# Optimization experiments

Hardware: AMD Instinct MI355X
Metric: run time of the kernel (lower is better)

## Reference

```python
import itertools
import jax, jax.numpy as jnp
import numpy as np

N_LEVELS = 16
N_FEATS = 2
LOG2_T = 19
BASE_RES = 16.0
FINEST_RES = 512.0
N_POINTS = 2 ** 21
MASK = np.uint32((1 << LOG2_T) - 1)
PRIMES = jnp.array([1, 2654435761, 805459861], dtype=jnp.uint32)
# 8 corner offsets of a voxel, [8, 3]
OFFSETS = jnp.array(list(itertools.product([0, 1], repeat=3)), dtype=jnp.int32)
BOX_MIN = jnp.zeros((3,), dtype=jnp.float32)
BOX_MAX = jnp.ones((3,), dtype=jnp.float32)
# per-level growth factor b = exp((log(finest)-log(base))/(L-1))
B_FACTOR = float(np.exp((np.log(FINEST_RES) - np.log(BASE_RES)) / (N_LEVELS - 1)))


def setup_inputs() -> dict:
    key = jax.random.key(0)
    k1, k2 = jax.random.split(key)
    x = jax.random.uniform(k1, (N_POINTS, 3), dtype=jnp.float32)
    # nn.init.uniform_(w, a=-1e-4, b=1e-4)
    tables = jax.random.uniform(k2, (N_LEVELS, 2 ** LOG2_T, N_FEATS),
                                dtype=jnp.float32, minval=-1e-4, maxval=1e-4)
    return {"x": x, "tables": tables}


def _hash(vidx):
    # vidx: [N, 8, 3] int32 voxel-corner integer coords
    v = vidx.astype(jnp.uint32)
    h = (v[..., 0] * PRIMES[0]) ^ (v[..., 1] * PRIMES[1]) ^ (v[..., 2] * PRIMES[2])
    return (h & MASK).astype(jnp.int32)  # [N, 8]


def _embed_level(x, table, resolution):
    # x: [N,3] float, table: [T,F], resolution: python float
    grid = (BOX_MAX - BOX_MIN) / resolution                      # [3]
    xc = jnp.clip(x, BOX_MIN, BOX_MAX)
    bl = jnp.floor((xc - BOX_MIN) / grid).astype(jnp.int32)      # [N,3]
    vmin = bl.astype(jnp.float32) * grid + BOX_MIN               # [N,3]
    vidx = bl[:, None, :] + OFFSETS[None, :, :]                  # [N,8,3]
    emb = table[_hash(vidx)]                                     # [N,8,F]
    rel = (xc - vmin) / grid                                     # [N,3]
    # trilinear weights: prod over dims of rel (offset=1) / 1-rel (offset=0)
    w = jnp.prod(jnp.where(OFFSETS[None, :, :] == 1,
                           rel[:, None, :], 1.0 - rel[:, None, :]), axis=-1)  # [N,8]
    return jnp.sum(w[..., None] * emb, axis=1)                   # [N,F]


def reference(x, tables):
    outs = []
    for i in range(N_LEVELS):
        resolution = float(np.floor(BASE_RES * B_FACTOR ** i))
        outs.append(_embed_level(x, tables[i], resolution))
    return jnp.concatenate(outs, axis=-1)  # [N, L*F]
```

## Files before the change

### kernel.cpp

```cpp
#include <hip/hip_runtime.h>
#include <stdint.h>


constexpr int kLevels = 16;
constexpr int kPoints = 1 << 21;
constexpr uint32_t kTableSize = 1u << 19;
constexpr uint32_t kMask = kTableSize - 1u;
constexpr size_t kPackedBytes = (size_t)kLevels * kTableSize * 4;
constexpr size_t kLvlOutBytes = (size_t)kLevels * kPoints * 4;

typedef float f32x4 __attribute__((ext_vector_type(4)));
typedef uint32_t u32x4 __attribute__((ext_vector_type(4)));

constexpr int kS0 = 17, kS1 = 21, kS2 = 26;
constexpr int kN0 = kS0 * kS0 * kS0;
constexpr int kN1 = kS1 * kS1 * kS1;
constexpr int kN2 = kS2 * kS2 * kS2;
constexpr int kB1 = kN0, kB2 = kN0 + kN1;
constexpr int kNDense = kN0 + kN1 + kN2;

constexpr int kG3 = 17 * 33 * 33;
constexpr int kG4 = 21 * 41 * 41;
constexpr int kG5 = 26 * 51 * 51;
constexpr int kG6 = 33 * 65 * 65;
constexpr int kGTot = kG3 + kG4 + kG5 + kG6;
constexpr size_t kX4Base3 = 131072;
constexpr size_t kX4Base4 = kX4Base3 + (size_t)kG3 * 16;
constexpr size_t kX4Base5 = kX4Base4 + (size_t)kG4 * 16;
constexpr size_t kX4Base6 = kX4Base5 + (size_t)kG5 * 16;

__constant__ float c_res[kLevels] = {
    16.f, 20.f, 25.f, 32.f, 40.f, 50.f, 64.f, 80.f,
    101.f, 128.f, 161.f, 203.f, 256.f, 322.f, 406.f, 512.f};

__device__ __forceinline__ uint32_t bf16_rtne_hi(float f) {
    uint32_t u = __float_as_uint(f);
    return (u + 0x7FFFu + ((u >> 16) & 1u)) >> 16;
}
__device__ __forceinline__ float bflo(uint32_t e) {
    return __uint_as_float(e << 16);
}
__device__ __forceinline__ float bfhi(uint32_t e) {
    return __uint_as_float(e & 0xFFFF0000u);
}

__global__ __launch_bounds__(256) void pack_tables_kernel(
    const float* __restrict__ tables, uint32_t* __restrict__ packed)
{
    const int i = blockIdx.x * 256 + threadIdx.x;
    const f32x4 v = reinterpret_cast<const f32x4*>(tables)[i];
    uint2 o;
    o.x = bf16_rtne_hi(v.x) | (bf16_rtne_hi(v.y) << 16);
    o.y = bf16_rtne_hi(v.z) | (bf16_rtne_hi(v.w) << 16);
    reinterpret_cast<uint2*>(packed)[i] = o;
}

template <int S, int LVL>
__device__ __forceinline__ void build_dense_one(
    int r, const float* __restrict__ tables, uint32_t* __restrict__ dst)
{
    const int bz = r % S;
    const int t = r / S;
    const int by = t % S;
    const int bx = t / S;
    const uint32_t h = ((uint32_t)bx ^ ((uint32_t)by * 2654435761u) ^
                        ((uint32_t)bz * 805459861u)) & kMask;
    const float* src = tables + (((size_t)LVL << 19) + h) * 2;
    dst[r] = bf16_rtne_hi(src[0]) | (bf16_rtne_hi(src[1]) << 16);
}

__global__ __launch_bounds__(256) void build_dense012_kernel(
    const float* __restrict__ tables, uint32_t* __restrict__ dense)
{
    const int idx = blockIdx.x * 256 + threadIdx.x;
    if (idx >= kNDense) return;
    if (idx < kB1)      build_dense_one<kS0, 0>(idx,       tables, dense);
    else if (idx < kB2) build_dense_one<kS1, 1>(idx - kB1, tables, dense + kB1);
    else                build_dense_one<kS2, 2>(idx - kB2, tables, dense + kB2);
}

template <int S, int LVL>
__device__ __forceinline__ void build_x4_one(
    int g, const uint32_t* __restrict__ packed, u32x4* __restrict__ dst)
{
    const int bz = g % S;
    const int t = g / S;
    const int by = t % S;
    const int gx = t / S;
    const uint32_t m = ((uint32_t)by * 2654435761u) ^
                       ((uint32_t)bz * 805459861u);
    const uint32_t e = (uint32_t)(gx * 2);
    const uint32_t* tab = packed + ((size_t)LVL << 19);
    u32x4 o;
    o.x = tab[((e + 0) ^ m) & kMask];
    o.y = tab[((e + 1) ^ m) & kMask];
    o.z = tab[((e + 2) ^ m) & kMask];
    o.w = tab[((e + 3) ^ m) & kMask];
    dst[g] = o;
}

__global__ __launch_bounds__(256) void build_x4_kernel(
    const uint32_t* __restrict__ packed, char* __restrict__ ws)
{
    const int g = blockIdx.x * 256 + threadIdx.x;
    if (g >= kGTot) return;
    if (g < kG3)
        build_x4_one<33, 3>(g, packed, (u32x4*)(ws + kX4Base3));
    else if (g < kG3 + kG4)
        build_x4_one<41, 4>(g - kG3, packed, (u32x4*)(ws + kX4Base4));
    else if (g < kG3 + kG4 + kG5)
        build_x4_one<51, 5>(g - kG3 - kG4, packed, (u32x4*)(ws + kX4Base5));
    else
        build_x4_one<65, 6>(g - kG3 - kG4 - kG5, packed, (u32x4*)(ws + kX4Base6));
}

template <int S, int BASE, int LVL>
__device__ __forceinline__ void eval_coarse(
    const uint32_t* __restrict__ lds, float px, float py, float pz, float r,
    uint32_t* __restrict__ lvl_out, int n)
{
    const float tx = px * r, ty = py * r, tz = pz * r;
    const float fx = floorf(tx), fy = floorf(ty), fz = floorf(tz);
    const int bx = (int)fx, by = (int)fy, bz = (int)fz;
    const float rx = tx - fx, ry = ty - fy, rz = tz - fz;
    const int c = BASE + (bx * S + by) * S + bz;
    const uint32_t e000 = lds[c],             e001 = lds[c + 1];
    const uint32_t e010 = lds[c + S],         e011 = lds[c + S + 1];
    const uint32_t e100 = lds[c + S * S],     e101 = lds[c + S * S + 1];
    const uint32_t e110 = lds[c + S * S + S], e111 = lds[c + S * S + S + 1];
    const float wx1 = rx, wx0 = 1.f - rx;
    const float wy1 = ry, wy0 = 1.f - ry;
    const float wz1 = rz, wz0 = 1.f - rz;
    float a0 = 0.f, a1 = 0.f;
    a0 = fmaf(wx0 * wy0 * wz0, bflo(e000), a0);
    a1 = fmaf(wx0 * wy0 * wz0, bfhi(e000), a1);
    a0 = fmaf(wx0 * wy0 * wz1, bflo(e001), a0);
    a1 = fmaf(wx0 * wy0 * wz1, bfhi(e001), a1);
    a0 = fmaf(wx0 * wy1 * wz0, bflo(e010), a0);
    a1 = fmaf(wx0 * wy1 * wz0, bfhi(e010), a1);
    a0 = fmaf(wx0 * wy1 * wz1, bflo(e011), a0);
    a1 = fmaf(wx0 * wy1 * wz1, bfhi(e011), a1);
    a0 = fmaf(wx1 * wy0 * wz0, bflo(e100), a0);
    a1 = fmaf(wx1 * wy0 * wz0, bfhi(e100), a1);
    a0 = fmaf(wx1 * wy0 * wz1, bflo(e101), a0);
    a1 = fmaf(wx1 * wy0 * wz1, bfhi(e101), a1);
    a0 = fmaf(wx1 * wy1 * wz0, bflo(e110), a0);
    a1 = fmaf(wx1 * wy1 * wz0, bfhi(e110), a1);
    a0 = fmaf(wx1 * wy1 * wz1, bflo(e111), a0);
    a1 = fmaf(wx1 * wy1 * wz1, bfhi(e111), a1);
    lvl_out[(size_t)LVL * kPoints + n] =
        bf16_rtne_hi(a0) | (bf16_rtne_hi(a1) << 16);
}

__global__ __launch_bounds__(512) void coarse_kernel(
    const float* __restrict__ x, const uint32_t* __restrict__ dense,
    uint32_t* __restrict__ lvl_out)
{
    __shared__ uint32_t s_tab[kNDense];
    for (int i = threadIdx.x; i < kNDense; i += 512) s_tab[i] = dense[i];
    __syncthreads();

    const int n0 = blockIdx.x * 2048 + threadIdx.x;
#pragma unroll
    for (int k = 0; k < 4; ++k) {
        const int n = n0 + k * 512;
        const float px = fminf(fmaxf(x[3 * n + 0], 0.0f), 1.0f);
        const float py = fminf(fmaxf(x[3 * n + 1], 0.0f), 1.0f);
        const float pz = fminf(fmaxf(x[3 * n + 2], 0.0f), 1.0f);
        eval_coarse<kS0, 0,   0>(s_tab, px, py, pz, 16.f, lvl_out, n);
        eval_coarse<kS1, kB1, 1>(s_tab, px, py, pz, 20.f, lvl_out, n);
        eval_coarse<kS2, kB2, 2>(s_tab, px, py, pz, 25.f, lvl_out, n);
    }
}

template <int S, int LVL>
__device__ __forceinline__ void eval_mid(
    const u32x4* __restrict__ tab, float px, float py, float pz, float r,
    uint32_t* __restrict__ lvl_out, int n)
{
    const float tx = px * r, ty = py * r, tz = pz * r;
    const float fx = floorf(tx), fy = floorf(ty), fz = floorf(tz);
    const int bx = (int)fx, by = (int)fy, bz = (int)fz;
    const float rx = tx - fx, ry = ty - fy, rz = tz - fz;
    const int gx = bx >> 1;
    const int par = bx & 1;
    const float wx1 = rx, wx0 = 1.f - rx;
    const float wy1 = ry, wy0 = 1.f - ry;
    const float wz1 = rz, wz0 = 1.f - rz;
    float a0 = 0.f, a1 = 0.f;
#pragma unroll
    for (int c = 0; c < 4; ++c) {
        const int gidx = (gx * S + (by + ((c >> 1) & 1))) * S + (bz + (c & 1));
        const u32x4 g = tab[gidx];
        const uint32_t lo = par ? g.y : g.x;
        const uint32_t hi = par ? g.z : g.y;
        const float wyz = ((c & 2) ? wy1 : wy0) * ((c & 1) ? wz1 : wz0);
        a0 = fmaf(wyz, fmaf(wx0, bflo(lo), wx1 * bflo(hi)), a0);
        a1 = fmaf(wyz, fmaf(wx0, bfhi(lo), wx1 * bfhi(hi)), a1);
    }
    lvl_out[(size_t)LVL * kPoints + n] =
        bf16_rtne_hi(a0) | (bf16_rtne_hi(a1) << 16);
}

__global__ __launch_bounds__(256) void mid_kernel(
    const float* __restrict__ x, const char* __restrict__ ws,
    uint32_t* __restrict__ lvl_out)
{
    const int b = blockIdx.x;
    const int sub = b >> 11;
    const int chunk = b & 2047;
    const int n0 = chunk * 1024 + threadIdx.x;
#pragma unroll
    for (int k = 0; k < 4; ++k) {
        const int n = n0 + k * 256;
        const float px = fminf(fmaxf(x[3 * n + 0], 0.0f), 1.0f);
        const float py = fminf(fmaxf(x[3 * n + 1], 0.0f), 1.0f);
        const float pz = fminf(fmaxf(x[3 * n + 2], 0.0f), 1.0f);
        if (sub == 0)
            eval_mid<33, 3>((const u32x4*)(ws + kX4Base3), px, py, pz, 32.f, lvl_out, n);
        else if (sub == 1)
            eval_mid<41, 4>((const u32x4*)(ws + kX4Base4), px, py, pz, 40.f, lvl_out, n);
        else if (sub == 2)
            eval_mid<51, 5>((const u32x4*)(ws + kX4Base5), px, py, pz, 50.f, lvl_out, n);
        else
            eval_mid<65, 6>((const u32x4*)(ws + kX4Base6), px, py, pz, 64.f, lvl_out, n);
    }
}

struct PtSt {
    float rx, ry, rz;
    uint32_t sel;
    uint2 p0, p1, p2, p3;
};

__device__ __forceinline__ void issue_pt(
    PtSt& st, const float* __restrict__ x, int n, float r,
    const uint32_t* __restrict__ tab)
{
    const float px = fminf(fmaxf(x[3 * n + 0], 0.f), 1.f);
    const float py = fminf(fmaxf(x[3 * n + 1], 0.f), 1.f);
    const float pz = fminf(fmaxf(x[3 * n + 2], 0.f), 1.f);
    const float tx = px * r, ty = py * r, tz = pz * r;
    const float fx = floorf(tx), fy = floorf(ty), fz = floorf(tz);
    const int bx = (int)fx, by = (int)fy, bz = (int)fz;
    st.rx = tx - fx;  st.ry = ty - fy;  st.rz = tz - fz;
    const uint32_t hy0 = (uint32_t)by * 2654435761u;
    const uint32_t hy1 = (uint32_t)(by + 1) * 2654435761u;
    const uint32_t hz0 = (uint32_t)bz * 805459861u;
    const uint32_t hz1 = (uint32_t)(bz + 1) * 805459861u;
    const uint32_t bxu = (uint32_t)bx, bx1 = bxu + 1u;
    const uint32_t m0 = hy0 ^ hz0, m1 = hy0 ^ hz1;
    const uint32_t m2 = hy1 ^ hz0, m3 = hy1 ^ hz1;
    if ((bx & 1) == 0) {
        const uint32_t h0 = (bxu ^ m0) & kMask;
        const uint32_t h1 = (bxu ^ m1) & kMask;
        const uint32_t h2 = (bxu ^ m2) & kMask;
        const uint32_t h3 = (bxu ^ m3) & kMask;
        st.sel = (h0 & 1u) | ((h1 & 1u) << 1) |
                 ((h2 & 1u) << 2) | ((h3 & 1u) << 3);
        st.p0 = *reinterpret_cast<const uint2*>(tab + (h0 & ~1u));
        st.p1 = *reinterpret_cast<const uint2*>(tab + (h1 & ~1u));
        st.p2 = *reinterpret_cast<const uint2*>(tab + (h2 & ~1u));
        st.p3 = *reinterpret_cast<const uint2*>(tab + (h3 & ~1u));
    } else {
        st.sel = 0u;
        st.p0.x = tab[(bxu ^ m0) & kMask];  st.p0.y = tab[(bx1 ^ m0) & kMask];
        st.p1.x = tab[(bxu ^ m1) & kMask];  st.p1.y = tab[(bx1 ^ m1) & kMask];
        st.p2.x = tab[(bxu ^ m2) & kMask];  st.p2.y = tab[(bx1 ^ m2) & kMask];
        st.p3.x = tab[(bxu ^ m3) & kMask];  st.p3.y = tab[(bx1 ^ m3) & kMask];
    }
}

__device__ __forceinline__ void consume_pt(
    const PtSt& st, uint32_t* __restrict__ w, int n)
{
    const float wx1 = st.rx, wx0 = 1.f - st.rx;
    const float wy1 = st.ry, wy0 = 1.f - st.ry;
    const float wz1 = st.rz, wz0 = 1.f - st.rz;
    const float w0 = wy0 * wz0, w1 = wy0 * wz1;
    const float w2 = wy1 * wz0, w3 = wy1 * wz1;
    const uint32_t e0 = (st.sel & 1u) ? st.p0.y : st.p0.x;
    const uint32_t f0 = (st.sel & 1u) ? st.p0.x : st.p0.y;
    const uint32_t e1 = (st.sel & 2u) ? st.p1.y : st.p1.x;
    const uint32_t f1 = (st.sel & 2u) ? st.p1.x : st.p1.y;
    const uint32_t e2 = (st.sel & 4u) ? st.p2.y : st.p2.x;
    const uint32_t f2 = (st.sel & 4u) ? st.p2.x : st.p2.y;
    const uint32_t e3 = (st.sel & 8u) ? st.p3.y : st.p3.x;
    const uint32_t f3 = (st.sel & 8u) ? st.p3.x : st.p3.y;
    float a0 = 0.f, a1 = 0.f;
    a0 = fmaf(w0, fmaf(wx0, bflo(e0), wx1 * bflo(f0)), a0);
    a1 = fmaf(w0, fmaf(wx0, bfhi(e0), wx1 * bfhi(f0)), a1);
    a0 = fmaf(w1, fmaf(wx0, bflo(e1), wx1 * bflo(f1)), a0);
    a1 = fmaf(w1, fmaf(wx0, bfhi(e1), wx1 * bfhi(f1)), a1);
    a0 = fmaf(w2, fmaf(wx0, bflo(e2), wx1 * bflo(f2)), a0);
    a1 = fmaf(w2, fmaf(wx0, bfhi(e2), wx1 * bfhi(f2)), a1);
    a0 = fmaf(w3, fmaf(wx0, bflo(e3), wx1 * bflo(f3)), a0);
    a1 = fmaf(w3, fmaf(wx0, bfhi(e3), wx1 * bfhi(f3)), a1);
    w[n] = bf16_rtne_hi(a0) | (bf16_rtne_hi(a1) << 16);
}

__global__ __launch_bounds__(256) void fine_kernel(
    const float* __restrict__ x,
    const uint32_t* __restrict__ packed,
    uint32_t* __restrict__ lvl_out)
{
    const int b = blockIdx.x;
    const int level = 7 + (b >> 11);
    const int chunk = b & 2047;

    const float r = c_res[level];
    const uint32_t* __restrict__ tab = packed + (size_t)level * kTableSize;
    uint32_t* __restrict__ w = lvl_out + (size_t)level * kPoints;

    const int n0 = chunk * 1024 + threadIdx.x;

    PtSt A, B;
    issue_pt(A, x, n0 + 0 * 256, r, tab);
    issue_pt(B, x, n0 + 1 * 256, r, tab);
    __builtin_amdgcn_sched_barrier(0);
    consume_pt(A, w, n0 + 0 * 256);
    __builtin_amdgcn_sched_barrier(0);
    issue_pt(A, x, n0 + 2 * 256, r, tab);
    __builtin_amdgcn_sched_barrier(0);
    consume_pt(B, w, n0 + 1 * 256);
    __builtin_amdgcn_sched_barrier(0);
    issue_pt(B, x, n0 + 3 * 256, r, tab);
    __builtin_amdgcn_sched_barrier(0);
    consume_pt(A, w, n0 + 2 * 256);
    __builtin_amdgcn_sched_barrier(0);
    consume_pt(B, w, n0 + 3 * 256);
}

__global__ __launch_bounds__(256) void untile_kernel(
    const uint32_t* __restrict__ lvl_out, float* __restrict__ out)
{
    const int n = blockIdx.x * 256 + threadIdx.x;
    float vals[2 * kLevels];
#pragma unroll
    for (int l = 0; l < kLevels; ++l) {
        const uint32_t u = lvl_out[(size_t)l * kPoints + n];
        vals[2 * l + 0] = bflo(u);
        vals[2 * l + 1] = bfhi(u);
    }
    float4* o4 = reinterpret_cast<float4*>(out + (size_t)n * (2 * kLevels));
#pragma unroll
    for (int kq = 0; kq < 8; ++kq) {
        o4[kq] = make_float4(vals[4 * kq + 0], vals[4 * kq + 1],
                             vals[4 * kq + 2], vals[4 * kq + 3]);
    }
}

__device__ __forceinline__ void eval_level(
    float px, float py, float pz, float r,
    const uint32_t* __restrict__ tab, float& a0, float& a1)
{
    const float tx = px * r, ty = py * r, tz = pz * r;
    const float fx = floorf(tx), fy = floorf(ty), fz = floorf(tz);
    const int bx = (int)fx, by = (int)fy, bz = (int)fz;
    const float rx = tx - fx, ry = ty - fy, rz = tz - fz;

    const uint32_t hx0 = (uint32_t)bx;
    const uint32_t hx1 = (uint32_t)(bx + 1);
    const uint32_t hy0 = (uint32_t)by * 2654435761u;
    const uint32_t hy1 = (uint32_t)(by + 1) * 2654435761u;
    const uint32_t hz0 = (uint32_t)bz * 805459861u;
    const uint32_t hz1 = (uint32_t)(bz + 1) * 805459861u;

    const float wx1 = rx, wx0 = 1.0f - rx;
    const float wy1 = ry, wy0 = 1.0f - ry;
    const float wz1 = rz, wz0 = 1.0f - rz;

    a0 = 0.0f; a1 = 0.0f;
#pragma unroll
    for (int c = 0; c < 8; ++c) {
        const uint32_t h = (((c & 4) ? hx1 : hx0) ^
                            ((c & 2) ? hy1 : hy0) ^
                            ((c & 1) ? hz1 : hz0)) & kMask;
        const uint32_t e = tab[h];
        const float w = ((c & 4) ? wx1 : wx0) *
                        ((c & 2) ? wy1 : wy0) *
                        ((c & 1) ? wz1 : wz0);
        a0 = fmaf(w, bflo(e), a0);
        a1 = fmaf(w, bfhi(e), a1);
    }
}

__global__ __launch_bounds__(256) void direct_kernel(
    const float* __restrict__ x,
    const float* __restrict__ tables,
    float* __restrict__ out)
{
    const int n = blockIdx.x * 256 + threadIdx.x;
    float px = fminf(fmaxf(x[3 * n + 0], 0.0f), 1.0f);
    float py = fminf(fmaxf(x[3 * n + 1], 0.0f), 1.0f);
    float pz = fminf(fmaxf(x[3 * n + 2], 0.0f), 1.0f);

    const float res_tab[kLevels] = {
        16.f, 20.f, 25.f, 32.f, 40.f, 50.f, 64.f, 80.f,
        101.f, 128.f, 161.f, 203.f, 256.f, 322.f, 406.f, 512.f};

    float acc[2 * kLevels];
#pragma unroll
    for (int l = 0; l < kLevels; ++l) {
        const float r = res_tab[l];
        const float tx = px * r, ty = py * r, tz = pz * r;
        const float fx = floorf(tx), fy = floorf(ty), fz = floorf(tz);
        const int bx = (int)fx, by = (int)fy, bz = (int)fz;
        const float rx = tx - fx, ry = ty - fy, rz = tz - fz;
        const uint32_t hx0 = (uint32_t)bx;
        const uint32_t hx1 = (uint32_t)(bx + 1);
        const uint32_t hy0 = (uint32_t)by * 2654435761u;
        const uint32_t hy1 = (uint32_t)(by + 1) * 2654435761u;
        const uint32_t hz0 = (uint32_t)bz * 805459861u;
        const uint32_t hz1 = (uint32_t)(bz + 1) * 805459861u;
        const float wx1 = rx, wx0 = 1.0f - rx;
        const float wy1 = ry, wy0 = 1.0f - ry;
        const float wz1 = rz, wz0 = 1.0f - rz;
        const float2* __restrict__ tab =
            reinterpret_cast<const float2*>(tables) + (size_t)l * kTableSize;
        float a0 = 0.0f, a1 = 0.0f;
#pragma unroll
        for (int c = 0; c < 8; ++c) {
            const uint32_t h = (((c & 4) ? hx1 : hx0) ^
                                ((c & 2) ? hy1 : hy0) ^
                                ((c & 1) ? hz1 : hz0)) & kMask;
            const float2 e = tab[h];
            const float w = ((c & 4) ? wx1 : wx0) *
                            ((c & 2) ? wy1 : wy0) *
                            ((c & 1) ? wz1 : wz0);
            a0 = fmaf(w, e.x, a0);
            a1 = fmaf(w, e.y, a1);
        }
        acc[2 * l + 0] = a0;
        acc[2 * l + 1] = a1;
    }
    float4* o4 = reinterpret_cast<float4*>(out + (size_t)n * (2 * kLevels));
#pragma unroll
    for (int kq = 0; kq < 8; ++kq) {
        o4[kq] = make_float4(acc[4 * kq + 0], acc[4 * kq + 1],
                             acc[4 * kq + 2], acc[4 * kq + 3]);
    }
}

__global__ __launch_bounds__(256) void direct_packed_kernel(
    const float* __restrict__ x,
    const uint32_t* __restrict__ packed,
    float* __restrict__ out)
{
    const int n = blockIdx.x * 256 + threadIdx.x;
    float px = fminf(fmaxf(x[3 * n + 0], 0.0f), 1.0f);
    float py = fminf(fmaxf(x[3 * n + 1], 0.0f), 1.0f);
    float pz = fminf(fmaxf(x[3 * n + 2], 0.0f), 1.0f);

    const float res_tab[kLevels] = {
        16.f, 20.f, 25.f, 32.f, 40.f, 50.f, 64.f, 80.f,
        101.f, 128.f, 161.f, 203.f, 256.f, 322.f, 406.f, 512.f};

    float acc[2 * kLevels];
#pragma unroll
    for (int l = 0; l < kLevels; ++l) {
        float a0, a1;
        eval_level(px, py, pz, res_tab[l],
                   packed + (size_t)l * kTableSize, a0, a1);
        acc[2 * l + 0] = a0;
        acc[2 * l + 1] = a1;
    }
    float4* o4 = reinterpret_cast<float4*>(out + (size_t)n * (2 * kLevels));
#pragma unroll
    for (int kq = 0; kq < 8; ++kq) {
        o4[kq] = make_float4(acc[4 * kq + 0], acc[4 * kq + 1],
                             acc[4 * kq + 2], acc[4 * kq + 3]);
    }
}

extern "C" void kernel_launch(void* const* d_in, const int* in_sizes, int n_in,
                              void* d_out, int out_size, void* d_ws, size_t ws_size,
                              hipStream_t stream) {
    const float* x = (const float*)d_in[0];
    const float* tables = (const float*)d_in[1];
    float* out = (float*)d_out;

    if (ws_size >= kPackedBytes + kLvlOutBytes) {
        char* ws = (char*)d_ws;
        uint32_t* packed = (uint32_t*)ws;
        uint32_t* lvl_out = (uint32_t*)(ws + kPackedBytes);
        uint32_t* dense012 = (uint32_t*)ws;

        hipLaunchKernelGGL(pack_tables_kernel,
                           dim3((kLevels * kTableSize / 2) / 256), dim3(256),
                           0, stream, tables, packed);
        hipLaunchKernelGGL(build_dense012_kernel,
                           dim3((kNDense + 255) / 256), dim3(256),
                           0, stream, tables, dense012);
        hipLaunchKernelGGL(build_x4_kernel,
                           dim3((kGTot + 255) / 256), dim3(256),
                           0, stream, packed, ws);
        hipLaunchKernelGGL(coarse_kernel, dim3(kPoints / 2048), dim3(512),
                           0, stream, x, dense012, lvl_out);
        hipLaunchKernelGGL(mid_kernel, dim3(4 * 2048), dim3(256),
                           0, stream, x, (const char*)ws, lvl_out);
        hipLaunchKernelGGL(fine_kernel, dim3(9 * 2048), dim3(256),
                           0, stream, x, packed, lvl_out);
        hipLaunchKernelGGL(untile_kernel, dim3(kPoints / 256), dim3(256),
                           0, stream, lvl_out, out);
    } else if (ws_size >= kPackedBytes) {
        uint32_t* packed = (uint32_t*)d_ws;
        hipLaunchKernelGGL(pack_tables_kernel,
                           dim3((kLevels * kTableSize / 2) / 256), dim3(256),
                           0, stream, tables, packed);
        hipLaunchKernelGGL(direct_packed_kernel, dim3(kPoints / 256), dim3(256),
                           0, stream, x, packed, out);
    } else {
        hipLaunchKernelGGL(direct_kernel, dim3(kPoints / 256), dim3(256),
                           0, stream, x, tables, out);
    }
}
```

Baseline: 572.3 us.

## Precompute full 8-corner voxel tables for mid levels and pack only fine levels

Replaces the x-pair grouped tables for levels 3-6 with a per-voxel layout that holds all 8 bf16-packed corner entries (32 bytes). Each point then needs two 16-byte loads instead of four gathers and parity selects. The voxel tables are built straight from the fp32 tables, so the pack kernel now converts only levels 7-15, which cuts pack traffic. The trade is larger mid-level tables (up to 65^3 x 32B, with level 6 placed inside unused lvl_out space), which add build cost and cache footprint.

Result: no change. 562.1 us (-1.8%).

```diff
diff --git a/kernel.cpp b/kernel.cpp
--- a/kernel.cpp
+++ b/kernel.cpp
@@ -19,15 +19,15 @@
 constexpr int kB1 = kN0, kB2 = kN0 + kN1;
 constexpr int kNDense = kN0 + kN1 + kN2;
 
-constexpr int kG3 = 17 * 33 * 33;
-constexpr int kG4 = 21 * 41 * 41;
-constexpr int kG5 = 26 * 51 * 51;
-constexpr int kG6 = 33 * 65 * 65;
-constexpr int kGTot = kG3 + kG4 + kG5 + kG6;
-constexpr size_t kX4Base3 = 131072;
-constexpr size_t kX4Base4 = kX4Base3 + (size_t)kG3 * 16;
-constexpr size_t kX4Base5 = kX4Base4 + (size_t)kG4 * 16;
-constexpr size_t kX4Base6 = kX4Base5 + (size_t)kG5 * 16;
+constexpr int kV3n = 33 * 33 * 33;
+constexpr int kV4n = 41 * 41 * 41;
+constexpr int kV5n = 51 * 51 * 51;
+constexpr int kV6n = 65 * 65 * 65;
+constexpr int kVTot = kV3n + kV4n + kV5n + kV6n;
+constexpr size_t kV3Base = 131072;
+constexpr size_t kV4Base = kV3Base + (size_t)kV3n * 32;
+constexpr size_t kV5Base = kV4Base + (size_t)kV4n * 32;
+constexpr size_t kV6Base = kPackedBytes + (size_t)7 * kPoints * 4;
 
 __constant__ float c_res[kLevels] = {
     16.f, 20.f, 25.f, 32.f, 40.f, 50.f, 64.f, 80.f,
@@ -45,9 +45,9 @@
 }
 
 __global__ __launch_bounds__(256) void pack_tables_kernel(
-    const float* __restrict__ tables, uint32_t* __restrict__ packed)
-{
-    const int i = blockIdx.x * 256 + threadIdx.x;
+    const float* __restrict__ tables, uint32_t* __restrict__ packed, int base)
+{
+    const int i = base + blockIdx.x * 256 + threadIdx.x;
     const f32x4 v = reinterpret_cast<const f32x4*>(tables)[i];
     uint2 o;
     o.x = bf16_rtne_hi(v.x) | (bf16_rtne_hi(v.y) << 16);
@@ -80,38 +80,45 @@
 }
 
 template <int S, int LVL>
-__device__ __forceinline__ void build_x4_one(
-    int g, const uint32_t* __restrict__ packed, u32x4* __restrict__ dst)
-{
-    const int bz = g % S;
-    const int t = g / S;
+__device__ __forceinline__ void build_vox_one(
+    int v, const float* __restrict__ tables, u32x4* __restrict__ dst)
+{
+    const int bz = v % S;
+    const int t = v / S;
     const int by = t % S;
-    const int gx = t / S;
-    const uint32_t m = ((uint32_t)by * 2654435761u) ^
-                       ((uint32_t)bz * 805459861u);
-    const uint32_t e = (uint32_t)(gx * 2);
-    const uint32_t* tab = packed + ((size_t)LVL << 19);
-    u32x4 o;
-    o.x = tab[((e + 0) ^ m) & kMask];
-    o.y = tab[((e + 1) ^ m) & kMask];
-    o.z = tab[((e + 2) ^ m) & kMask];
-    o.w = tab[((e + 3) ^ m) & kMask];
-    dst[g] = o;
-}
-
-__global__ __launch_bounds__(256) void build_x4_kernel(
-    const uint32_t* __restrict__ packed, char* __restrict__ ws)
-{
-    const int g = blockIdx.x * 256 + threadIdx.x;
-    if (g >= kGTot) return;
-    if (g < kG3)
-        build_x4_one<33, 3>(g, packed, (u32x4*)(ws + kX4Base3));
-    else if (g < kG3 + kG4)
-        build_x4_one<41, 4>(g - kG3, packed, (u32x4*)(ws + kX4Base4));
-    else if (g < kG3 + kG4 + kG5)
-        build_x4_one<51, 5>(g - kG3 - kG4, packed, (u32x4*)(ws + kX4Base5));
+    const int bx = t / S;
+    const float* tab = tables + (((size_t)LVL << 19) * 2);
+    uint32_t e[8];
+#pragma unroll
+    for (int c = 0; c < 8; ++c) {
+        const uint32_t xx = (uint32_t)(bx + ((c >> 2) & 1));
+        const uint32_t yy = (uint32_t)(by + ((c >> 1) & 1));
+        const uint32_t zz = (uint32_t)(bz + (c & 1));
+        const uint32_t h = (xx ^ (yy * 2654435761u) ^ (zz * 805459861u)) & kMask;
+        const float* src = tab + (size_t)h * 2;
+        e[c] = bf16_rtne_hi(src[0]) | (bf16_rtne_hi(src[1]) << 16);
+    }
+    u32x4 q0, q1;
+    q0.x = e[0]; q0.y = e[1]; q0.z = e[2]; q0.w = e[3];
+    q1.x = e[4]; q1.y = e[5]; q1.z = e[6]; q1.w = e[7];
+    dst[2 * v + 0] = q0;
+    dst[2 * v + 1] = q1;
+}
+
+__global__ __launch_bounds__(256) void build_vox_kernel(
+    const float* __restrict__ tables, char* __restrict__ ws)
+{
+    const int v = blockIdx.x * 256 + threadIdx.x;
+    if (v >= kVTot) return;
+    if (v < kV3n)
+        build_vox_one<33, 3>(v, tables, (u32x4*)(ws + kV3Base));
+    else if (v < kV3n + kV4n)
+        build_vox_one<41, 4>(v - kV3n, tables, (u32x4*)(ws + kV4Base));
+    else if (v < kV3n + kV4n + kV5n)
+        build_vox_one<51, 5>(v - kV3n - kV4n, tables, (u32x4*)(ws + kV5Base));
     else
-        build_x4_one<65, 6>(g - kG3 - kG4 - kG5, packed, (u32x4*)(ws + kX4Base6));
+        build_vox_one<65, 6>(v - kV3n - kV4n - kV5n, tables,
+                             (u32x4*)(ws + kV6Base));
 }
 
 template <int S, int BASE, int LVL>
@@ -173,31 +180,40 @@
     }
 }
 
-template <int S, int LVL>
-__device__ __forceinline__ void eval_mid(
-    const u32x4* __restrict__ tab, float px, float py, float pz, float r,
+template <int R, int LVL>
+__device__ __forceinline__ void eval_vox(
+    const u32x4* __restrict__ V, float px, float py, float pz,
     uint32_t* __restrict__ lvl_out, int n)
 {
+    const float r = (float)R;
     const float tx = px * r, ty = py * r, tz = pz * r;
     const float fx = floorf(tx), fy = floorf(ty), fz = floorf(tz);
     const int bx = (int)fx, by = (int)fy, bz = (int)fz;
     const float rx = tx - fx, ry = ty - fy, rz = tz - fz;
-    const int gx = bx >> 1;
-    const int par = bx & 1;
+    constexpr int S = R + 1;
+    const int idx = (bx * S + by) * S + bz;
+    const u32x4 q0 = V[2 * idx + 0];
+    const u32x4 q1 = V[2 * idx + 1];
     const float wx1 = rx, wx0 = 1.f - rx;
     const float wy1 = ry, wy0 = 1.f - ry;
     const float wz1 = rz, wz0 = 1.f - rz;
     float a0 = 0.f, a1 = 0.f;
-#pragma unroll
-    for (int c = 0; c < 4; ++c) {
-        const int gidx = (gx * S + (by + ((c >> 1) & 1))) * S + (bz + (c & 1));
-        const u32x4 g = tab[gidx];
-        const uint32_t lo = par ? g.y : g.x;
-        const uint32_t hi = par ? g.z : g.y;
-        const float wyz = ((c & 2) ? wy1 : wy0) * ((c & 1) ? wz1 : wz0);
-        a0 = fmaf(wyz, fmaf(wx0, bflo(lo), wx1 * bflo(hi)), a0);
-        a1 = fmaf(wyz, fmaf(wx0, bfhi(lo), wx1 * bfhi(hi)), a1);
-    }
+    a0 = fmaf(wx0 * wy0 * wz0, bflo(q0.x), a0);
+    a1 = fmaf(wx0 * wy0 * wz0, bfhi(q0.x), a1);
+    a0 = fmaf(wx0 * wy0 * wz1, bflo(q0.y), a0);
+    a1 = fmaf(wx0 * wy0 * wz1, bfhi(q0.y), a1);
+    a0 = fmaf(wx0 * wy1 * wz0, bflo(q0.z), a0);
+    a1 = fmaf(wx0 * wy1 * wz0, bfhi(q0.z), a1);
+    a0 = fmaf(wx0 * wy1 * wz1, bflo(q0.w), a0);
+    a1 = fmaf(wx0 * wy1 * wz1, bfhi(q0.w), a1);
+    a0 = fmaf(wx1 * wy0 * wz0, bflo(q1.x), a0);
+    a1 = fmaf(wx1 * wy0 * wz0, bfhi(q1.x), a1);
+    a0 = fmaf(wx1 * wy0 * wz1, bflo(q1.y), a0);
+    a1 = fmaf(wx1 * wy0 * wz1, bfhi(q1.y), a1);
+    a0 = fmaf(wx1 * wy1 * wz0, bflo(q1.z), a0);
+    a1 = fmaf(wx1 * wy1 * wz0, bfhi(q1.z), a1);
+    a0 = fmaf(wx1 * wy1 * wz1, bflo(q1.w), a0);
+    a1 = fmaf(wx1 * wy1 * wz1, bfhi(q1.w), a1);
     lvl_out[(size_t)LVL * kPoints + n] =
         bf16_rtne_hi(a0) | (bf16_rtne_hi(a1) << 16);
 }
@@ -217,13 +233,13 @@
         const float py = fminf(fmaxf(x[3 * n + 1], 0.0f), 1.0f);
         const float pz = fminf(fmaxf(x[3 * n + 2], 0.0f), 1.0f);
         if (sub == 0)
-            eval_mid<33, 3>((const u32x4*)(ws + kX4Base3), px, py, pz, 32.f, lvl_out, n);
+            eval_vox<32, 3>((const u32x4*)(ws + kV3Base), px, py, pz, lvl_out, n);
         else if (sub == 1)
-            eval_mid<41, 4>((const u32x4*)(ws + kX4Base4), px, py, pz, 40.f, lvl_out, n);
+            eval_vox<40, 4>((const u32x4*)(ws + kV4Base), px, py, pz, lvl_out, n);
         else if (sub == 2)
-            eval_mid<51, 5>((const u32x4*)(ws + kX4Base5), px, py, pz, 50.f, lvl_out, n);
+            eval_vox<50, 5>((const u32x4*)(ws + kV5Base), px, py, pz, lvl_out, n);
         else
-            eval_mid<65, 6>((const u32x4*)(ws + kX4Base6), px, py, pz, 64.f, lvl_out, n);
+            eval_vox<64, 6>((const u32x4*)(ws + kV6Base), px, py, pz, lvl_out, n);
     }
 }
 
@@ -487,14 +503,14 @@
         uint32_t* dense012 = (uint32_t*)ws;
 
         hipLaunchKernelGGL(pack_tables_kernel,
-                           dim3((kLevels * kTableSize / 2) / 256), dim3(256),
-                           0, stream, tables, packed);
+                           dim3((9 << 19) / 2 / 256), dim3(256),
+                           0, stream, tables, packed, (7 << 19) / 2);
         hipLaunchKernelGGL(build_dense012_kernel,
                            dim3((kNDense + 255) / 256), dim3(256),
                            0, stream, tables, dense012);
-        hipLaunchKernelGGL(build_x4_kernel,
-                           dim3((kGTot + 255) / 256), dim3(256),
-                           0, stream, packed, ws);
+        hipLaunchKernelGGL(build_vox_kernel,
+                           dim3((kVTot + 255) / 256), dim3(256),
+                           0, stream, tables, ws);
         hipLaunchKernelGGL(coarse_kernel, dim3(kPoints / 2048), dim3(512),
                            0, stream, x, dense012, lvl_out);
         hipLaunchKernelGGL(mid_kernel, dim3(4 * 2048), dim3(256),
@@ -507,7 +523,7 @@
         uint32_t* packed = (uint32_t*)d_ws;
         hipLaunchKernelGGL(pack_tables_kernel,
                            dim3((kLevels * kTableSize / 2) / 256), dim3(256),
-                           0, stream, tables, packed);
+                           0, stream, tables, packed, 0);
         hipLaunchKernelGGL(direct_packed_kernel, dim3(kPoints / 256), dim3(256),
                            0, stream, x, packed, out);
     } else {
```
